# Optimization experiments

Hardware: AMD Instinct MI355X
Metric: run time of the kernel (lower is better)

Reference implementation:

```python
import jax, jax.numpy as jnp
import numpy as np

# S4D diagonal SSM kernel generation (disc='zoh', real_type='exp', no state, rate=1.0)
H = 768      # model width (number of SSM copies)
N = 64       # state size per SSM
CH = 1       # kernel channels
NSSM = 768   # n_ssm == H -> repeat = 1 (untied)
L_VAL = 2048 # target kernel length


def setup_inputs() -> dict:
    key = jax.random.key(0)
    k_dt, k_C = jax.random.split(key, 2)
    # dt log-uniform in [1e-3, 1e-1]
    log_dt = np.log(1e-3) + jax.random.uniform(k_dt, (H,), dtype=jnp.float32) * (np.log(1e-1) - np.log(1e-3))
    # B = 1 + 0j  (standard S4D init), stored as real/imag pair
    B_ri = jnp.concatenate([jnp.ones((NSSM, N, 1), jnp.float32), jnp.zeros((NSSM, N, 1), jnp.float32)], axis=-1)
    # A = -0.5 + i*pi*n  (S4D-Lin); real_type='exp' -> inv_A_real = log(-A_real) = log(0.5)
    inv_A_real = jnp.full((NSSM, N), np.log(0.5), dtype=jnp.float32)
    A_imag = jnp.tile(np.pi * jnp.arange(N, dtype=jnp.float32)[None, :], (NSSM, 1))
    C_ri = jax.random.normal(k_C, (CH, H, N, 2), dtype=jnp.float32)
    return {"log_dt": log_dt, "B_ri": B_ri, "inv_A_real": inv_A_real,
            "A_imag": A_imag, "C_ri": C_ri, "L": L_VAL}


def reference(log_dt, B_ri, inv_A_real, A_imag, C_ri, L):
    dt = jnp.exp(log_dt)                               # (H,)
    A = -jnp.exp(inv_A_real) + 1j * A_imag             # (n_ssm, N) complex
    rep = H // A.shape[0]
    A = jnp.tile(A, (rep, 1))                          # (H, N)
    B = B_ri[..., 0] + 1j * B_ri[..., 1]               # (n_ssm, N)
    B = jnp.tile(B, (rep, 1))[None]                    # (1, H, N)
    C = C_ri[..., 0] + 1j * C_ri[..., 1]               # (CH, H, N)
    C = (B[:, None, :, :] * C).reshape(-1, H, N)       # (CH, H, N)
    dtA = A * dt[:, None]                              # (H, N)
    # ZOH discretization of C
    C = C * (jnp.exp(dtA) - 1.0) / A                   # (CH, H, N)
    # log-Vandermonde: K[c,h,l] = 2*Re( sum_n C[c,h,n] * exp(dtA[h,n] * l) )
    ell = jnp.arange(L, dtype=jnp.float32)
    V = jnp.exp(dtA[:, :, None] * ell)                 # (H, N, L) complex64 -- dominant intermediate
    K = 2.0 * jnp.einsum('chn,hnl->chl', C, V).real    # (CH, H, L)
    return K.astype(jnp.float32)
```

## Files before the change

### kernel.cpp

```cpp
#include <hip/hip_runtime.h>


typedef float v2f __attribute__((ext_vector_type(2)));

#define H_DIM 768
#define N_DIM 64
#define L_DIM 2048
#define TPB   512
#define LTH   64
#define LCH   32
#define NBITS 6

__global__ __launch_bounds__(TPB, 4) void s4d_gen_kernel(
    const float* __restrict__ log_dt,
    const float* __restrict__ B_ri,
    const float* __restrict__ inv_A_real,
    const float* __restrict__ A_imag,
    const float* __restrict__ C_ri,
    float* __restrict__ out)
{
    __shared__ v2f  sW[N_DIM];
    __shared__ v2f  sG[N_DIM];
    __shared__ v2f  sT[NBITS][N_DIM];
    __shared__ v2f  sC1p[N_DIM / 2];
    __shared__ v2f  sNC2p[N_DIM / 2];
    __shared__ float sRed[4][LCH][LTH];

    const int h  = blockIdx.x;
    const int t  = threadIdx.x;
    const int nb = t >> 6;
    const int tl = t & 63;

    if (t < N_DIM) {
        const int n   = t;
        const int idx = h * N_DIM + n;
        const float dt = expf(log_dt[h]);
        const float Ar = -expf(inv_A_real[idx]);
        const float Ai = A_imag[idx];
        const float e  = expf(Ar * dt);
        float s, c;
        sincosf(Ai * dt, &s, &c);
        const float wr = e * c, wi = e * s;
        const float inv = 1.0f / (Ar * Ar + Ai * Ai);
        const float nr = wr - 1.0f, ni = wi;
        const float qr = (nr * Ar + ni * Ai) * inv;
        const float qi = (ni * Ar - nr * Ai) * inv;
        const float Br = B_ri[2 * idx], Bi = B_ri[2 * idx + 1];
        const float Cr = C_ri[2 * idx], Ci = C_ri[2 * idx + 1];
        const float BCr = Br * Cr - Bi * Ci;
        const float BCi = Br * Ci + Bi * Cr;
        sG[n] = (v2f){2.0f * (BCr * qr - BCi * qi),
                      2.0f * (BCr * qi + BCi * qr)};
        sW[n] = (v2f){wr, wi};
        ((float*)sC1p)[n]  = 2.0f * wr;
        ((float*)sNC2p)[n] = -(wr * wr + wi * wi);
        float pr = wr, pi = wi;
        #pragma unroll
        for (int k = 0; k < 5; ++k) { float t2 = pr*pr - pi*pi; pi = 2.0f*pr*pi; pr = t2; }
        #pragma unroll
        for (int k = 0; k < NBITS; ++k) {
            sT[k][n] = (v2f){pr, pi};
            float t2 = pr*pr - pi*pi; pi = 2.0f*pr*pi; pr = t2;
        }
    }
    __syncthreads();

    v2f acc2[LCH];
    #pragma unroll
    for (int j = 0; j < LCH; ++j) acc2[j] = (v2f){0.0f, 0.0f};

    const int nbase = nb * 8;

    for (int pp = 0; pp < 2; ++pp) {
        const int na = nbase + 4 * pp;
        const int nc = na + 2;

        v2f uA0 = sG[na], uA1 = sG[na + 1];
        v2f uB0 = sG[nc], uB1 = sG[nc + 1];
        #pragma unroll
        for (int k = 0; k < NBITS; ++k) {
            const bool b = (tl >> k) & 1;
            const v2f tA0 = sT[k][na],     tA1 = sT[k][na + 1];
            const v2f tB0 = sT[k][nc],     tB1 = sT[k][nc + 1];
            const float mA0r = b ? tA0.x : 1.0f, mA0i = b ? tA0.y : 0.0f;
            const float mA1r = b ? tA1.x : 1.0f, mA1i = b ? tA1.y : 0.0f;
            const float mB0r = b ? tB0.x : 1.0f, mB0i = b ? tB0.y : 0.0f;
            const float mB1r = b ? tB1.x : 1.0f, mB1i = b ? tB1.y : 0.0f;
            float r0 = uA0.x*mA0r - uA0.y*mA0i; uA0.y = uA0.x*mA0i + uA0.y*mA0r; uA0.x = r0;
            float r1 = uA1.x*mA1r - uA1.y*mA1i; uA1.y = uA1.x*mA1i + uA1.y*mA1r; uA1.x = r1;
            float r2 = uB0.x*mB0r - uB0.y*mB0i; uB0.y = uB0.x*mB0i + uB0.y*mB0r; uB0.x = r2;
            float r3 = uB1.x*mB1r - uB1.y*mB1i; uB1.y = uB1.x*mB1i + uB1.y*mB1r; uB1.x = r3;
        }
        const v2f wA0 = sW[na], wA1 = sW[na + 1];
        const v2f wB0 = sW[nc], wB1 = sW[nc + 1];
        v2f s0A = (v2f){uA0.x, uA1.x};
        v2f s1A = (v2f){wA0.x*uA0.x - wA0.y*uA0.y, wA1.x*uA1.x - wA1.y*uA1.y};
        v2f s0B = (v2f){uB0.x, uB1.x};
        v2f s1B = (v2f){wB0.x*uB0.x - wB0.y*uB0.y, wB1.x*uB1.x - wB1.y*uB1.y};
        const v2f c1A  = sC1p[na >> 1],  c1B  = sC1p[nc >> 1];
        const v2f nc2A = sNC2p[na >> 1], nc2B = sNC2p[nc >> 1];

        #pragma unroll
        for (int j = 0; j < LCH; ++j) {
            acc2[j] += s0A;
            acc2[j] += s0B;
            v2f tA = c1A * s1A;
            v2f nA = __builtin_elementwise_fma(nc2A, s0A, tA);
            s0A = s1A; s1A = nA;
            v2f tB = c1B * s1B;
            v2f nB = __builtin_elementwise_fma(nc2B, s0B, tB);
            s0B = s1B; s1B = nB;
        }
    }

    float acc[LCH];
    #pragma unroll
    for (int j = 0; j < LCH; ++j) acc[j] = acc2[j].x + acc2[j].y;

    if (nb >= 4) {
        #pragma unroll
        for (int j = 0; j < LCH; ++j) sRed[nb - 4][j][tl] = acc[j];
    }
    __syncthreads();
    if (nb < 4) {
        #pragma unroll
        for (int j = 0; j < LCH; ++j) acc[j] += sRed[nb][j][tl];
    }
    __syncthreads();
    if (nb == 2 || nb == 3) {
        #pragma unroll
        for (int j = 0; j < LCH; ++j) sRed[nb - 2][j][tl] = acc[j];
    }
    __syncthreads();
    if (nb < 2) {
        #pragma unroll
        for (int j = 0; j < LCH; ++j) acc[j] += sRed[nb][j][tl];
    }
    __syncthreads();
    if (nb == 1) {
        #pragma unroll
        for (int j = 0; j < LCH; ++j) sRed[0][j][tl] = acc[j];
    }
    __syncthreads();
    if (nb == 0) {
        #pragma unroll
        for (int j = 0; j < LCH; ++j) acc[j] += sRed[0][j][tl];
        float* op = out + (size_t)h * L_DIM + tl * LCH;
        #pragma unroll
        for (int j = 0; j < LCH; j += 4) {
            *reinterpret_cast<float4*>(op + j) =
                make_float4(acc[j], acc[j + 1], acc[j + 2], acc[j + 3]);
        }
    }
}

extern "C" void kernel_launch(void* const* d_in, const int* in_sizes, int n_in,
                              void* d_out, int out_size, void* d_ws, size_t ws_size,
                              hipStream_t stream) {
    const float* log_dt     = (const float*)d_in[0];
    const float* B_ri       = (const float*)d_in[1];
    const float* inv_A_real = (const float*)d_in[2];
    const float* A_imag     = (const float*)d_in[3];
    const float* C_ri       = (const float*)d_in[4];
    float* out = (float*)d_out;
    hipLaunchKernelGGL(s4d_gen_kernel, dim3(H_DIM), dim3(TPB), 0, stream,
                       log_dt, B_ri, inv_A_real, A_imag, C_ri, out);
}
```

Measured before the change: 76.56 us.

## Compute chunk-start powers via direct exp2/sin/cos and halve block size

Instead of a binary-power product over six precomputed squarings, each thread computes w^(32*tl) directly from the reduced phase (computed in double on setup) and log2 magnitude, using hardware fract/sin/cos/exp2 intrinsics. G and G*w are folded into the seeds, so only the real part is formed. The block shrinks to 256 threads, each handling 16 state modes across 4 outer iterations, which removes one level of the shared-memory reduction. Hardware transcendental approximations may lose accuracy, and the longer per-thread loop gives fewer waves per block.

```diff
diff --git a/kernel.cpp b/kernel.cpp
--- a/kernel.cpp
+++ b/kernel.cpp
@@ -1,4 +1,5 @@
 #include <hip/hip_runtime.h>
+#include <math.h>
 
 
 typedef float v2f __attribute__((ext_vector_type(2)));
@@ -6,12 +7,11 @@
 #define H_DIM 768
 #define N_DIM 64
 #define L_DIM 2048
-#define TPB   512
+#define TPB   256
 #define LTH   64
 #define LCH   32
-#define NBITS 6
 
-__global__ __launch_bounds__(TPB, 4) void s4d_gen_kernel(
+__global__ __launch_bounds__(TPB, 3) void s4d_gen_kernel(
     const float* __restrict__ log_dt,
     const float* __restrict__ B_ri,
     const float* __restrict__ inv_A_real,
@@ -19,12 +19,11 @@
     const float* __restrict__ C_ri,
     float* __restrict__ out)
 {
-    __shared__ v2f  sW[N_DIM];
-    __shared__ v2f  sG[N_DIM];
-    __shared__ v2f  sT[NBITS][N_DIM];
-    __shared__ v2f  sC1p[N_DIM / 2];
-    __shared__ v2f  sNC2p[N_DIM / 2];
-    __shared__ float sRed[4][LCH][LTH];
+    __shared__ float4 sP0[N_DIM];
+    __shared__ float4 sP1[N_DIM];
+    __shared__ v2f    sC1p[N_DIM / 2];
+    __shared__ v2f    sNC2p[N_DIM / 2];
+    __shared__ float  sRed[2][LCH][LTH];
 
     const int h  = blockIdx.x;
     const int t  = threadIdx.x;
@@ -37,9 +36,11 @@
         const float dt = expf(log_dt[h]);
         const float Ar = -expf(inv_A_real[idx]);
         const float Ai = A_imag[idx];
-        const float e  = expf(Ar * dt);
+        const float dtAr = Ar * dt;
+        const float dtAi = Ai * dt;
+        const float e  = expf(dtAr);
         float s, c;
-        sincosf(Ai * dt, &s, &c);
+        sincosf(dtAi, &s, &c);
         const float wr = e * c, wi = e * s;
         const float inv = 1.0f / (Ar * Ar + Ai * Ai);
         const float nr = wr - 1.0f, ni = wi;
@@ -49,19 +50,15 @@
         const float Cr = C_ri[2 * idx], Ci = C_ri[2 * idx + 1];
         const float BCr = Br * Cr - Bi * Ci;
         const float BCi = Br * Ci + Bi * Cr;
-        sG[n] = (v2f){2.0f * (BCr * qr - BCi * qi),
-                      2.0f * (BCr * qi + BCi * qr)};
-        sW[n] = (v2f){wr, wi};
+        const float Gr = 2.0f * (BCr * qr - BCi * qi);
+        const float Gi = 2.0f * (BCr * qi + BCi * qr);
+        const double revs32 = (double)dtAi * (32.0 / (2.0 * M_PI));
+        const float  r32f   = (float)(revs32 - floor(revs32));
+        const float  l2m32  = dtAr * (32.0f * 1.4426950408889634f);
+        sP0[n] = make_float4(r32f, l2m32, Gr, Gi);
+        sP1[n] = make_float4(Gr * wr - Gi * wi, Gr * wi + Gi * wr, 0.0f, 0.0f);
         ((float*)sC1p)[n]  = 2.0f * wr;
         ((float*)sNC2p)[n] = -(wr * wr + wi * wi);
-        float pr = wr, pi = wi;
-        #pragma unroll
-        for (int k = 0; k < 5; ++k) { float t2 = pr*pr - pi*pi; pi = 2.0f*pr*pi; pr = t2; }
-        #pragma unroll
-        for (int k = 0; k < NBITS; ++k) {
-            sT[k][n] = (v2f){pr, pi};
-            float t2 = pr*pr - pi*pi; pi = 2.0f*pr*pi; pr = t2;
-        }
     }
     __syncthreads();
 
@@ -69,34 +66,45 @@
     #pragma unroll
     for (int j = 0; j < LCH; ++j) acc2[j] = (v2f){0.0f, 0.0f};
 
-    const int nbase = nb * 8;
+    const int   nbase = nb * 16;
+    const float tlf   = (float)tl;
 
-    for (int pp = 0; pp < 2; ++pp) {
+    #pragma unroll 1
+    for (int pp = 0; pp < 4; ++pp) {
         const int na = nbase + 4 * pp;
         const int nc = na + 2;
 
-        v2f uA0 = sG[na], uA1 = sG[na + 1];
-        v2f uB0 = sG[nc], uB1 = sG[nc + 1];
-        #pragma unroll
-        for (int k = 0; k < NBITS; ++k) {
-            const bool b = (tl >> k) & 1;
-            const v2f tA0 = sT[k][na],     tA1 = sT[k][na + 1];
-            const v2f tB0 = sT[k][nc],     tB1 = sT[k][nc + 1];
-            const float mA0r = b ? tA0.x : 1.0f, mA0i = b ? tA0.y : 0.0f;
-            const float mA1r = b ? tA1.x : 1.0f, mA1i = b ? tA1.y : 0.0f;
-            const float mB0r = b ? tB0.x : 1.0f, mB0i = b ? tB0.y : 0.0f;
-            const float mB1r = b ? tB1.x : 1.0f, mB1i = b ? tB1.y : 0.0f;
-            float r0 = uA0.x*mA0r - uA0.y*mA0i; uA0.y = uA0.x*mA0i + uA0.y*mA0r; uA0.x = r0;
-            float r1 = uA1.x*mA1r - uA1.y*mA1i; uA1.y = uA1.x*mA1i + uA1.y*mA1r; uA1.x = r1;
-            float r2 = uB0.x*mB0r - uB0.y*mB0i; uB0.y = uB0.x*mB0i + uB0.y*mB0r; uB0.x = r2;
-            float r3 = uB1.x*mB1r - uB1.y*mB1i; uB1.y = uB1.x*mB1i + uB1.y*mB1r; uB1.x = r3;
-        }
-        const v2f wA0 = sW[na], wA1 = sW[na + 1];
-        const v2f wB0 = sW[nc], wB1 = sW[nc + 1];
-        v2f s0A = (v2f){uA0.x, uA1.x};
-        v2f s1A = (v2f){wA0.x*uA0.x - wA0.y*uA0.y, wA1.x*uA1.x - wA1.y*uA1.y};
-        v2f s0B = (v2f){uB0.x, uB1.x};
-        v2f s1B = (v2f){wB0.x*uB0.x - wB0.y*uB0.y, wB1.x*uB1.x - wB1.y*uB1.y};
+        const float4 pA0 = sP0[na], pA1 = sP0[na + 1];
+        const float4 pB0 = sP0[nc], pB1 = sP0[nc + 1];
+        const float4 qA0 = sP1[na], qA1 = sP1[na + 1];
+        const float4 qB0 = sP1[nc], qB1 = sP1[nc + 1];
+
+        const float fA0 = __builtin_amdgcn_fractf(pA0.x * tlf);
+        const float fA1 = __builtin_amdgcn_fractf(pA1.x * tlf);
+        const float fB0 = __builtin_amdgcn_fractf(pB0.x * tlf);
+        const float fB1 = __builtin_amdgcn_fractf(pB1.x * tlf);
+        const float snA0 = __builtin_amdgcn_sinf(fA0), csA0 = __builtin_amdgcn_cosf(fA0);
+        const float snA1 = __builtin_amdgcn_sinf(fA1), csA1 = __builtin_amdgcn_cosf(fA1);
+        const float snB0 = __builtin_amdgcn_sinf(fB0), csB0 = __builtin_amdgcn_cosf(fB0);
+        const float snB1 = __builtin_amdgcn_sinf(fB1), csB1 = __builtin_amdgcn_cosf(fB1);
+        const float mA0 = __builtin_amdgcn_exp2f(pA0.y * tlf);
+        const float mA1 = __builtin_amdgcn_exp2f(pA1.y * tlf);
+        const float mB0 = __builtin_amdgcn_exp2f(pB0.y * tlf);
+        const float mB1 = __builtin_amdgcn_exp2f(pB1.y * tlf);
+        const float urA0 = mA0 * csA0, uiA0 = mA0 * snA0;
+        const float urA1 = mA1 * csA1, uiA1 = mA1 * snA1;
+        const float urB0 = mB0 * csB0, uiB0 = mB0 * snB0;
+        const float urB1 = mB1 * csB1, uiB1 = mB1 * snB1;
+
+        v2f s0A = (v2f){fmaf(pA0.z, urA0, -(pA0.w * uiA0)),
+                        fmaf(pA1.z, urA1, -(pA1.w * uiA1))};
+        v2f s1A = (v2f){fmaf(qA0.x, urA0, -(qA0.y * uiA0)),
+                        fmaf(qA1.x, urA1, -(qA1.y * uiA1))};
+        v2f s0B = (v2f){fmaf(pB0.z, urB0, -(pB0.w * uiB0)),
+                        fmaf(pB1.z, urB1, -(pB1.w * uiB1))};
+        v2f s1B = (v2f){fmaf(qB0.x, urB0, -(qB0.y * uiB0)),
+                        fmaf(qB1.x, urB1, -(qB1.y * uiB1))};
+
         const v2f c1A  = sC1p[na >> 1],  c1B  = sC1p[nc >> 1];
         const v2f nc2A = sNC2p[na >> 1], nc2B = sNC2p[nc >> 1];
 
@@ -117,17 +125,7 @@
     #pragma unroll
     for (int j = 0; j < LCH; ++j) acc[j] = acc2[j].x + acc2[j].y;
 
-    if (nb >= 4) {
-        #pragma unroll
-        for (int j = 0; j < LCH; ++j) sRed[nb - 4][j][tl] = acc[j];
-    }
-    __syncthreads();
-    if (nb < 4) {
-        #pragma unroll
-        for (int j = 0; j < LCH; ++j) acc[j] += sRed[nb][j][tl];
-    }
-    __syncthreads();
-    if (nb == 2 || nb == 3) {
+    if (nb >= 2) {
         #pragma unroll
         for (int j = 0; j < LCH; ++j) sRed[nb - 2][j][tl] = acc[j];
     }
```

New measurement: 72.87 us. -4.8%, faster.
